# Kernel optimization log

Measured on AMD Instinct MI355X. Metric: run time of the kernel, lower is better.

Reference implementation:

```python
import jax, jax.numpy as jnp
import numpy as np

# Straight-through-estimator round (round_pass in the original code)
def _round_ste(x):
    return x + jax.lax.stop_gradient(jnp.round(x) - x)

INPUT_QMAX = 127.0   # 2**(input_bit-1)-1,  input_bit=8
WEIGHT_QMAX = 127.0  # 2**(weight_bit-1)-1, weight_bit=8
OUT_RANGE = 127.0    # 2**(output_bit-1)-1, output_bit=8


def setup_inputs() -> dict:
    key = jax.random.key(0)
    k0, k1, k2 = jax.random.split(key, 3)
    B, Cin, Cout, H, W, K = 16, 320, 320, 64, 64, 3
    x = jax.random.normal(k0, (B, Cin, H, W), dtype=jnp.float32)
    weight = jax.random.normal(k1, (Cout, Cin, K, K), dtype=jnp.float32) * 0.05
    bias = jax.random.normal(k2, (Cout,), dtype=jnp.float32) * 0.1
    # LSQ learned scalar step sizes (cloned from conv_lsq in the original)
    step_x = jnp.float32(0.02)
    step_w = jnp.float32(0.002)
    step_b = jnp.float32(0.01)
    # Bit_shift_layer scale: shift conv accumulator down into output_bit range
    shift_scale = jnp.float32(2.0 ** -7)
    return {"x": x, "weight": weight, "bias": bias, "step_x": step_x,
            "step_w": step_w, "step_b": step_b, "shift_scale": shift_scale}


def reference(x, weight, bias, step_x, step_w, step_b, shift_scale):
    # --- lsq_quant_input (isint=True): x_int in [-127,127], x_scale = 1/step ---
    x_int = jnp.clip(_round_ste(x / step_x), -INPUT_QMAX, INPUT_QMAX)
    x_scale = 1.0 / step_x
    # --- lsq_quant_weight (isint=True) ---
    w_int = jnp.clip(_round_ste(weight / step_w), -WEIGHT_QMAX, WEIGHT_QMAX)
    w_scale = 1.0 / step_w
    # --- Conv2d_int: integer-valued conv (no bias) ---
    y_int = jax.lax.conv_general_dilated(
        x_int, w_int, window_strides=(1, 1), padding=((1, 1), (1, 1)),
        dimension_numbers=("NCHW", "OIHW", "NCHW"))
    # --- mvm_result_shift: bit-shift accumulator into output range ---
    y_shift = jnp.clip(_round_ste(y_int * shift_scale), -OUT_RANGE, OUT_RANGE)
    # --- lsq_quant_bias (isint=False): dequantized bias ---
    b_deq = jnp.clip(_round_ste(bias / step_b), -OUT_RANGE, OUT_RANGE) * step_b
    # --- bias requant to output int scale, add, clamp (fused epilogue) ---
    b_int8 = jnp.clip(_round_ste(b_deq * shift_scale * x_scale * w_scale),
                      -OUT_RANGE, OUT_RANGE)
    y_shift_dmac = jnp.clip(y_shift + b_int8[None, :, None, None],
                            -OUT_RANGE, OUT_RANGE)
    # module returns y_shift_DMAC (the integer-valued clamped output)
    return y_shift_dmac
```

## Files before the change

### kernel.cpp

```cpp
#include <hip/hip_runtime.h>

typedef int v4i __attribute__((ext_vector_type(4)));

#define QMAX 127.0f

#define XQ_BYTES 22302720
#define WQ_BYTES 921600

__device__ __forceinline__ float clampf(float v, float lo, float hi) {
    return fminf(fmaxf(v, lo), hi);
}

__device__ __forceinline__ void gload_lds16(const char* g, char* l) {
    __builtin_amdgcn_global_load_lds(
        (const __attribute__((address_space(1))) void*)g,
        (__attribute__((address_space(3))) void*)l, 16, 0, 0);
}

__device__ __forceinline__ v4i mfma_i8(v4i a, v4i b, v4i c) {
    return __builtin_amdgcn_mfma_i32_16x16x64_i8(a, b, c, 0, 0, 0);
}

__global__ __launch_bounds__(256) void quant_x_kernel(
    const float* __restrict__ x, const float* __restrict__ step_p,
    char* __restrict__ xq)
{
    __shared__ float F[64 * 65];
    const int t   = threadIdx.x;
    const int ci0 = blockIdx.x * 64;
    const int h   = blockIdx.y;
    const int b   = blockIdx.z;
    const float step = *step_p;

    {
        const int r = t >> 4, c = (t & 15) * 4;
        const float* src = x + (((size_t)(b * 320 + ci0) * 64 + h) * 64);
#pragma unroll
        for (int i = 0; i < 4; ++i) {
            const int row = r + i * 16;
            float4 v = *(const float4*)(src + (size_t)row * 4096 + c);
            *(float4*)&F[row * 65 + c] = v;
        }
    }
    __syncthreads();

    {
        const int w  = t & 63;
        const int cg = t >> 6;
        int dws[4];
#pragma unroll
        for (int j = 0; j < 4; ++j) {
            int word = 0;
#pragma unroll
            for (int k2 = 0; k2 < 4; ++k2) {
                int ci = cg * 16 + j * 4 + k2;
                float v = F[ci * 65 + w];
                int xi = (int)clampf(rintf(v / step), -QMAX, QMAX);
                word |= (xi & 0xFF) << (8 * k2);
            }
            dws[j] = word;
        }
        v4i pk = { dws[0], dws[1], dws[2], dws[3] };
        size_t off = ((size_t)(b * 66 + (h + 1)) * 66 + (w + 1)) * 320 + ci0 + cg * 16;
        *(v4i*)&xq[off] = pk;
    }
}

__global__ __launch_bounds__(256) void prep_kernel(
    const float* __restrict__ w, const float* __restrict__ bias,
    const float* __restrict__ step_w_p, const float* __restrict__ step_b_p,
    const float* __restrict__ step_x_p, const float* __restrict__ shift_p,
    char* __restrict__ wq2, char* __restrict__ xq, float* __restrict__ bi)
{
    const int bid = blockIdx.x;
    if (bid < 3600) {
        const int tid = bid * 256 + threadIdx.x;
        const float step = *step_w_p;
        const int p    = tid / 102400;
        const int r    = tid - p * 102400;
        const int c5   = r / 20480;
        const int r2   = r - c5 * 20480;
        const int cog  = r2 >> 10;
        const int r3   = r2 & 1023;
        const int lane = r3 >> 4, j = r3 & 15;
        const int co = cog * 16 + (lane & 15);
        const int ci = c5 * 64 + (lane >> 4) * 16 + j;
        float v = w[(size_t)co * 2880 + ci * 9 + p];
        int q = (int)clampf(rintf(v / step), -QMAX, QMAX);
        wq2[tid] = (char)q;
    } else if (bid < 3925) {
        int tid = (bid - 3600) * 256 + threadIdx.x;
        if (tid < 83200) {
            int b = tid / 5200;
            int r = tid - b * 5200;
            int px = r / 20;
            int ck = (r - px * 20) * 16;
            int row, col;
            if (px < 66)       { row = 0;  col = px; }
            else if (px < 132) { row = 65; col = px - 66; }
            else { int e = px - 132; row = 1 + (e >> 1); col = (e & 1) * 65; }
            size_t off = ((size_t)(b * 66 + row) * 66 + col) * 320 + ck;
            v4i z = {0, 0, 0, 0};
            *(v4i*)&xq[off] = z;
        }
    } else {
        const float step_b = *step_b_p;
        const float xs = 1.0f / *step_x_p;
        const float ws = 1.0f / *step_w_p;
        const float shift = *shift_p;
#pragma unroll
        for (int co = threadIdx.x; co < 320; co += 256) {
            float b_deq = clampf(rintf(bias[co] / step_b), -QMAX, QMAX) * step_b;
            float v = ((b_deq * shift) * xs) * ws;
            bi[co] = clampf(rintf(v), -QMAX, QMAX);
        }
    }
}

template<int ROWS, int WAVES>
__global__ __launch_bounds__(WAVES * 64, 2) void conv_mfma_kernel(
    const char* __restrict__ xq, const char* __restrict__ wq2,
    const float* __restrict__ bi, const float* __restrict__ shift_p,
    float* __restrict__ out)
{
    extern __shared__ __align__(16) char lds[];
    char* B_lds = lds;
    char* A_lds = lds + (ROWS + 2) * 66 * 64;

    const int t   = threadIdx.x;
    const int bx  = blockIdx.x;
    const int co0 = bx * 64;
    const int ptile = blockIdx.y;
    constexpr int TPI = 64 / ROWS;
    const int b  = ptile / TPI;
    const int h0 = (ptile % TPI) * ROWS;

    const int wave = t >> 6, lane = t & 63;
    const int quad = lane >> 4, l15 = lane & 15;

    const char* xbase = xq + ((size_t)(b * 66 + h0) * 66) * 320;
    constexpr int BCHUNKS = (ROWS + 2) * 66 * 4;

    v4i acc[4][8] = {};

    for (int c5 = 0; c5 < 5; ++c5) {
        const int ci0 = c5 * 64;

        for (int c = t; c < BCHUNKS; c += WAVES * 64) {
            int px = c >> 2;
            int ck = (c & 3) << 4;
            v4i v = *(const v4i*)&xbase[(size_t)px * 320 + ci0 + ck];
            *(v4i*)&B_lds[px * 64 + (ck ^ ((((px >> 1) & 3)) << 4))] = v;
        }
        for (int seg = wave; seg < 36; seg += WAVES) {
            int p = seg >> 2, cog = seg & 3;
            const char* g = wq2 + (size_t)p * 102400
                            + ((size_t)(c5 * 20 + bx * 4 + cog)) * 1024
                            + (size_t)lane * 16;
            gload_lds16(g, &A_lds[seg * 1024]);
        }
        __syncthreads();

#pragma unroll
        for (int p = 0; p < 9; ++p) {
            const int dh = p / 3, dw = p - dh * 3;
            v4i a[4];
#pragma unroll
            for (int cs = 0; cs < 4; ++cs)
                a[cs] = *(const v4i*)&A_lds[(p * 4 + cs) * 1024 + lane * 16];
#pragma unroll
            for (int half = 0; half < 2; ++half) {
                const int prow = wave * 2 + half + dh;
#pragma unroll
                for (int i = 0; i < 4; ++i) {
                    const int px = prow * 66 + i * 16 + l15 + dw;
                    v4i bf = *(const v4i*)&B_lds[px * 64 +
                              ((quad << 4) ^ ((((px >> 1) & 3)) << 4))];
#pragma unroll
                    for (int cs = 0; cs < 4; ++cs)
                        acc[cs][half * 4 + i] = mfma_i8(a[cs], bf, acc[cs][half * 4 + i]);
                }
            }
        }
        __syncthreads();
    }

    const float shift = *shift_p;
#pragma unroll
    for (int cs = 0; cs < 4; ++cs) {
#pragma unroll
        for (int reg = 0; reg < 4; ++reg) {
            const int co = co0 + cs * 16 + quad * 4 + reg;
            const float bv = bi[co];
#pragma unroll
            for (int half = 0; half < 2; ++half) {
                const int h = h0 + wave * 2 + half;
                float* orow = out + (((size_t)(b * 320 + co) * 64) + h) * 64;
#pragma unroll
                for (int i = 0; i < 4; ++i) {
                    float y  = (float)acc[cs][half * 4 + i][reg];
                    float ys = clampf(rintf(y * shift), -QMAX, QMAX);
                    orow[i * 16 + l15] = clampf(ys + bv, -QMAX, QMAX);
                }
            }
        }
    }
}

extern "C" void kernel_launch(void* const* d_in, const int* in_sizes, int n_in,
                              void* d_out, int out_size, void* d_ws, size_t ws_size,
                              hipStream_t stream) {
    const float* x      = (const float*)d_in[0];
    const float* w      = (const float*)d_in[1];
    const float* bias   = (const float*)d_in[2];
    const float* step_x = (const float*)d_in[3];
    const float* step_w = (const float*)d_in[4];
    const float* step_b = (const float*)d_in[5];
    const float* shift  = (const float*)d_in[6];
    float* out = (float*)d_out;

    char*  xq  = (char*)d_ws;
    char*  wq2 = xq + XQ_BYTES;
    float* bi  = (float*)(wq2 + WQ_BYTES);

    quant_x_kernel<<<dim3(5, 64, 16), 256, 0, stream>>>(x, step_x, xq);
    prep_kernel<<<3926, 256, 0, stream>>>(w, bias, step_w, step_b, step_x, shift,
                                          wq2, xq, bi);

    const int lds_big = (8 + 2) * 66 * 64 + 36864;
    hipError_t e = hipFuncSetAttribute(
        reinterpret_cast<const void*>(&conv_mfma_kernel<8, 4>),
        hipFuncAttributeMaxDynamicSharedMemorySize, lds_big);
    if (e == hipSuccess) {
        conv_mfma_kernel<8, 4><<<dim3(5, 128), 256, lds_big, stream>>>(
            xq, wq2, bi, shift, out);
    } else {
        (void)hipGetLastError();
        const int lds_small = (4 + 2) * 66 * 64 + 36864;
        conv_mfma_kernel<4, 2><<<dim3(5, 256), 128, lds_small, stream>>>(
            xq, wq2, bi, shift, out);
    }
}
```

Before: 236.7 us.

## Pre-swizzle activations in global memory, load via direct-to-LDS, read weights from global

The quantize kernel now processes all 320 channels per block and writes the activation tile with the LDS XOR swizzle already applied in global memory. This lets the conv kernel copy it straight into LDS with global_load_lds instead of going through registers. Weights are no longer staged in LDS but read from global memory (expected to hit L2), which cuts LDS use to a static 42 KB and allows three blocks per CU. The cost is more global and L2 weight traffic inside the inner loop, plus extra serialized loop iterations in the quantize kernel.

After: 497.8 us. +110.3%, slower.

```diff
diff --git a/kernel.cpp b/kernel.cpp
--- a/kernel.cpp
+++ b/kernel.cpp
@@ -26,44 +26,48 @@
     char* __restrict__ xq)
 {
     __shared__ float F[64 * 65];
-    const int t   = threadIdx.x;
-    const int ci0 = blockIdx.x * 64;
-    const int h   = blockIdx.y;
-    const int b   = blockIdx.z;
+    const int t = threadIdx.x;
+    const int h = blockIdx.x;
+    const int b = blockIdx.y;
     const float step = *step_p;
-
-    {
-        const int r = t >> 4, c = (t & 15) * 4;
-        const float* src = x + (((size_t)(b * 320 + ci0) * 64 + h) * 64);
-#pragma unroll
-        for (int i = 0; i < 4; ++i) {
-            const int row = r + i * 16;
-            float4 v = *(const float4*)(src + (size_t)row * 4096 + c);
-            *(float4*)&F[row * 65 + c] = v;
-        }
-    }
-    __syncthreads();
-
-    {
-        const int w  = t & 63;
-        const int cg = t >> 6;
+    const int w  = t >> 2;
+    const int cg = t & 3;
+    v4i vals[5];
+
+    for (int c5 = 0; c5 < 5; ++c5) {
+        {
+            const int r = t >> 4, c = (t & 15) * 4;
+            const float* src = x + (((size_t)(b * 320 + c5 * 64) * 64 + h) * 64);
+#pragma unroll
+            for (int i = 0; i < 4; ++i) {
+                const int row = r + i * 16;
+                *(float4*)&F[row * 65 + c] =
+                    *(const float4*)(src + (size_t)row * 4096 + c);
+            }
+        }
+        __syncthreads();
         int dws[4];
 #pragma unroll
         for (int j = 0; j < 4; ++j) {
             int word = 0;
 #pragma unroll
-            for (int k2 = 0; k2 < 4; ++k2) {
-                int ci = cg * 16 + j * 4 + k2;
-                float v = F[ci * 65 + w];
+            for (int k = 0; k < 4; ++k) {
+                float v = F[(cg * 16 + j * 4 + k) * 65 + w];
                 int xi = (int)clampf(rintf(v / step), -QMAX, QMAX);
-                word |= (xi & 0xFF) << (8 * k2);
+                word |= (xi & 0xFF) << (8 * k);
             }
             dws[j] = word;
         }
-        v4i pk = { dws[0], dws[1], dws[2], dws[3] };
-        size_t off = ((size_t)(b * 66 + (h + 1)) * 66 + (w + 1)) * 320 + ci0 + cg * 16;
-        *(v4i*)&xq[off] = pk;
-    }
+        vals[c5] = (v4i){dws[0], dws[1], dws[2], dws[3]};
+        __syncthreads();
+    }
+
+    const int col = w + 1;
+    const int key = (col >> 1) & 3;
+    char* base = xq + ((size_t)(b * 66 + (h + 1)) * 66 + col) * 320;
+#pragma unroll
+    for (int c5 = 0; c5 < 5; ++c5)
+        *(v4i*)(base + c5 * 64 + (((cg ^ key)) << 4)) = vals[c5];
 }
 
 __global__ __launch_bounds__(256) void prep_kernel(
@@ -117,47 +121,34 @@
     }
 }
 
-template<int ROWS, int WAVES>
-__global__ __launch_bounds__(WAVES * 64, 2) void conv_mfma_kernel(
+__global__ __launch_bounds__(256, 3) void conv_mfma_kernel(
     const char* __restrict__ xq, const char* __restrict__ wq2,
     const float* __restrict__ bi, const float* __restrict__ shift_p,
     float* __restrict__ out)
 {
-    extern __shared__ __align__(16) char lds[];
-    char* B_lds = lds;
-    char* A_lds = lds + (ROWS + 2) * 66 * 64;
+    __shared__ __attribute__((aligned(16))) char B_lds[42240];
 
     const int t   = threadIdx.x;
     const int bx  = blockIdx.x;
     const int co0 = bx * 64;
     const int ptile = blockIdx.y;
-    constexpr int TPI = 64 / ROWS;
-    const int b  = ptile / TPI;
-    const int h0 = (ptile % TPI) * ROWS;
+    const int b  = ptile >> 3;
+    const int h0 = (ptile & 7) * 8;
 
     const int wave = t >> 6, lane = t & 63;
     const int quad = lane >> 4, l15 = lane & 15;
 
     const char* xbase = xq + ((size_t)(b * 66 + h0) * 66) * 320;
-    constexpr int BCHUNKS = (ROWS + 2) * 66 * 4;
 
     v4i acc[4][8] = {};
 
     for (int c5 = 0; c5 < 5; ++c5) {
         const int ci0 = c5 * 64;
-
-        for (int c = t; c < BCHUNKS; c += WAVES * 64) {
-            int px = c >> 2;
-            int ck = (c & 3) << 4;
-            v4i v = *(const v4i*)&xbase[(size_t)px * 320 + ci0 + ck];
-            *(v4i*)&B_lds[px * 64 + (ck ^ ((((px >> 1) & 3)) << 4))] = v;
-        }
-        for (int seg = wave; seg < 36; seg += WAVES) {
-            int p = seg >> 2, cog = seg & 3;
-            const char* g = wq2 + (size_t)p * 102400
-                            + ((size_t)(c5 * 20 + bx * 4 + cog)) * 1024
-                            + (size_t)lane * 16;
-            gload_lds16(g, &A_lds[seg * 1024]);
+        const char* wp = wq2 + (c5 * 20 + bx * 4) * 1024 + lane * 16;
+
+        for (int c = t; c < 2640; c += 256) {
+            const char* g = xbase + (c >> 2) * 320 + ci0 + ((c & 3) << 4);
+            gload_lds16(g, &B_lds[(c - lane) * 16]);
         }
         __syncthreads();
 
@@ -167,18 +158,20 @@
             v4i a[4];
 #pragma unroll
             for (int cs = 0; cs < 4; ++cs)
-                a[cs] = *(const v4i*)&A_lds[(p * 4 + cs) * 1024 + lane * 16];
+                a[cs] = *(const v4i*)(wp + p * 102400 + cs * 1024);
 #pragma unroll
             for (int half = 0; half < 2; ++half) {
                 const int prow = wave * 2 + half + dh;
 #pragma unroll
                 for (int i = 0; i < 4; ++i) {
-                    const int px = prow * 66 + i * 16 + l15 + dw;
-                    v4i bf = *(const v4i*)&B_lds[px * 64 +
-                              ((quad << 4) ^ ((((px >> 1) & 3)) << 4))];
+                    const int col = i * 16 + l15 + dw;
+                    const int key = (col >> 1) & 3;
+                    v4i bf = *(const v4i*)&B_lds[(prow * 66 + col) * 64 +
+                                                 ((quad ^ key) << 4)];
 #pragma unroll
                     for (int cs = 0; cs < 4; ++cs)
-                        acc[cs][half * 4 + i] = mfma_i8(a[cs], bf, acc[cs][half * 4 + i]);
+                        acc[cs][half * 4 + i] =
+                            mfma_i8(a[cs], bf, acc[cs][half * 4 + i]);
                 }
             }
         }
@@ -223,21 +216,8 @@
     char*  wq2 = xq + XQ_BYTES;
     float* bi  = (float*)(wq2 + WQ_BYTES);
 
-    quant_x_kernel<<<dim3(5, 64, 16), 256, 0, stream>>>(x, step_x, xq);
+    quant_x_kernel<<<dim3(64, 16), 256, 0, stream>>>(x, step_x, xq);
     prep_kernel<<<3926, 256, 0, stream>>>(w, bias, step_w, step_b, step_x, shift,
                                           wq2, xq, bi);
-
-    const int lds_big = (8 + 2) * 66 * 64 + 36864;
-    hipError_t e = hipFuncSetAttribute(
-        reinterpret_cast<const void*>(&conv_mfma_kernel<8, 4>),
-        hipFuncAttributeMaxDynamicSharedMemorySize, lds_big);
-    if (e == hipSuccess) {
-        conv_mfma_kernel<8, 4><<<dim3(5, 128), 256, lds_big, stream>>>(
-            xq, wq2, bi, shift, out);
-    } else {
-        (void)hipGetLastError();
-        const int lds_small = (4 + 2) * 66 * 64 + 36864;
-        conv_mfma_kernel<4, 2><<<dim3(5, 256), 128, lds_small, stream>>>(
-            xq, wq2, bi, shift, out);
-    }
-}
+    conv_mfma_kernel<<<dim3(5, 128), 256, 0, stream>>>(xq, wq2, bi, shift, out);
+}
```
